# Kernel tuning notes

Measured on AMD Instinct MI355X. Metric: run time of the kernel, lower is better.

Reference implementation:

```python
import math
import jax, jax.numpy as jnp
import numpy as np

B, N, D, H, R = 2, 2048, 1024, 16, 32
DK = D // H  # 64


def _alibi_slopes(n_heads):
    def pow2slopes(n):
        start = 2 ** (-(2 ** (-(math.log2(n) - 3))))
        return [start * (start ** i) for i in range(n)]
    if math.log2(n_heads).is_integer():
        vals = pow2slopes(n_heads)
    else:
        closest = 2 ** math.floor(math.log2(n_heads))
        vals = pow2slopes(closest)
        vals += pow2slopes(2 * closest)[0::2][: n_heads - closest]
    return np.asarray(vals, dtype=np.float32)


def _alibi_bias(n_heads, n_tokens):
    # bias[h, i, j] = -slope[h] * max(j - i, 0)
    i = np.arange(n_tokens)[:, None]
    j = np.arange(n_tokens)[None, :]
    dist = np.clip(j - i, 0, None).astype(np.float32)
    return jnp.asarray(-_alibi_slopes(n_heads)[:, None, None] * dist)  # [H, N, N]


def setup_inputs() -> dict:
    key = jax.random.key(0)
    ks = jax.random.split(key, 6)
    s = 0.02
    return {
        "x": jax.random.normal(ks[0], (B, N, D), dtype=jnp.float32),
        "mask": jnp.zeros((1, 1, N, N), dtype=jnp.float32),
        "W_q": jax.random.normal(ks[1], (D, D), dtype=jnp.float32) * s,
        "W_k": jax.random.normal(ks[2], (D, D), dtype=jnp.float32) * s,
        "W_v": jax.random.normal(ks[3], (D, D), dtype=jnp.float32) * s,
        "U": jax.random.normal(ks[4], (DK, R), dtype=jnp.float32) * (1.0 / math.sqrt(DK)),
        "W_proj": jax.random.normal(ks[5], (D, D), dtype=jnp.float32) * s,
        "rel_bias_tokens": N,
    }


def reference(x, mask, W_q, W_k, W_v, U, W_proj, rel_bias_tokens):
    b, n, d = x.shape
    dk = U.shape[0]
    h = d // dk
    # q/k: Linear (no bias) -> split heads -> low-rank projection via U: [b,h,n,r]
    q = jnp.einsum("bnhd,dr->bhnr", (x @ W_q.T).reshape(b, n, h, dk), U)
    k = jnp.einsum("bnhd,dr->bhnr", (x @ W_k.T).reshape(b, n, h, dk), U)
    v = (x @ W_v.T).reshape(b, n, h, dk).transpose(0, 2, 1, 3)  # [b,h,n,dk]
    # note: scale uses sqrt(dk), not sqrt(r) (custom scale from the module)
    att = jnp.einsum("bhnr,bhmr->bhnm", q, k) / math.sqrt(dk)
    bias = _alibi_bias(h, rel_bias_tokens)  # [h, N_total, N_total]
    att = att + bias[None, :, -n:, :] + mask
    p = jax.nn.softmax(att, axis=-1)
    z = jnp.einsum("bhnm,bhmd->bnhd", p, v).reshape(b, n, h * dk)
    return z @ W_proj.T  # dropout is identity at inference
```

## Files before the change

kernel.cpp:

```cpp
#include <hip/hip_runtime.h>
#include <cstdint>

#define DEV __device__ __forceinline__

typedef __bf16 bf16x8 __attribute__((ext_vector_type(8)));
typedef float f32x4 __attribute__((ext_vector_type(4)));
typedef unsigned short u16x4 __attribute__((ext_vector_type(4)));
typedef unsigned short u16x8 __attribute__((ext_vector_type(8)));
typedef float f32x4v __attribute__((ext_vector_type(4)));

DEV unsigned short f2bf(float f) {
  union { float f; unsigned int u; } v; v.f = f;
  unsigned int r = v.u + 0x7fffu + ((v.u >> 16) & 1u);
  return (unsigned short)(r >> 16);
}

DEV void gl2lds16(const void* g, void* l) {
  __builtin_amdgcn_global_load_lds(
      (const __attribute__((address_space(1))) void*)g,
      (__attribute__((address_space(3))) void*)l, 16, 0, 0);
}

DEV bf16x8 ld8(const unsigned short* p) { return *(const bf16x8*)p; }


__global__ __launch_bounds__(256) void prep(
    const float* __restrict__ x, const float* __restrict__ Wp,
    const float* __restrict__ Wv, const float* __restrict__ Wq,
    const float* __restrict__ Wk, const float* __restrict__ U,
    unsigned short* __restrict__ xb, unsigned short* __restrict__ Wpb,
    unsigned short* __restrict__ Wcat) {
  __shared__ float Us[64 * 32];
  const int bx = blockIdx.x, t = threadIdx.x;
  if (bx < 6144) {
    const float* s; unsigned short* d; int i;
    if (bx < 4096)      { s = x;  d = xb;               i = bx * 256 + t; }
    else if (bx < 5120) { s = Wp; d = Wpb;              i = (bx - 4096) * 256 + t; }
    else                { s = Wv; d = Wcat + 1024*1024; i = (bx - 5120) * 256 + t; }
    f32x4v f = ((const f32x4v*)s)[i];
    u16x4 u;
    u[0] = f2bf(f[0]); u[1] = f2bf(f[1]); u[2] = f2bf(f[2]); u[3] = f2bf(f[3]);
    ((u16x4*)d)[i] = u;
  } else {
    ((f32x4v*)Us)[t] = ((const f32x4v*)U)[t];
    ((f32x4v*)Us)[t + 256] = ((const f32x4v*)U)[t + 256];
    __syncthreads();
    int gid = (bx - 6144) * 256 + t;
    int d = gid & 1023;
    int tmp = gid >> 10;
    int rq = tmp & 7, hh = (tmp >> 3) & 15, qk = tmp >> 7;
    const float* W = qk ? Wk : Wq;
    const float* wp = W + (size_t)(hh * 64) * 1024 + d;
    f32x4v acc = {0.f, 0.f, 0.f, 0.f};
    #pragma unroll 8
    for (int dk = 0; dk < 64; dk++) {
      float wv = wp[(size_t)dk * 1024];
      acc += (*(const f32x4v*)(Us + dk * 32 + rq * 4)) * wv;
    }
    float sc = qk ? 1.0f : 0.18033688011112042f;
    int orow = qk * 512 + hh * 32 + rq * 4;
    #pragma unroll
    for (int i = 0; i < 4; i++)
      Wcat[(size_t)(orow + i) * 1024 + d] = f2bf(acc[i] * sc);
  }
}


template <int OUTF32, int VW, int BM>
__global__ __launch_bounds__(512, 1) void gemm256(
    const unsigned short* __restrict__ A, const unsigned short* __restrict__ Bt,
    void* __restrict__ Cout, unsigned short* __restrict__ Vt,
    int nbx, int Nc, int K) {
  constexpr int MI = BM / 64;
  constexpr int NL = BM / 64 + 2;
  __shared__ __align__(16) unsigned short As[3][BM * 64];
  __shared__ __align__(16) unsigned short Bs[3][128 * 64];
  const int t = threadIdx.x;
  const int w = t >> 6, lane = t & 63;
  const int quad = lane >> 4, l15 = lane & 15;

  const int per = gridDim.x >> 3;
  const int f = blockIdx.x;
  const int wgid = (f & 7) * per + (f >> 3);
  const int by = wgid / nbx, bx = wgid - by * nbx;
  const int row0 = by * BM, col0 = bx * 128;

  const int wr = (w >> 1) * (BM / 4), wc = (w & 1) * 64;

  f32x4 acc[MI][4];
  #pragma unroll
  for (int i = 0; i < MI; i++)
    #pragma unroll
    for (int j = 0; j < 4; j++) acc[i][j] = (f32x4){0.f, 0.f, 0.f, 0.f};

  const int srow = t >> 3;
  const int chnk = t & 7;
  const int swz = (chnk ^ (srow & 7)) * 8;
  const unsigned short* ga = A + (size_t)(row0 + srow) * K + swz;
  const unsigned short* gb = Bt + (size_t)(col0 + srow) * K + swz;
  const int ldsb = w * 512;

  #pragma unroll
  for (int q = 0; q < MI; q++) gl2lds16(ga + (size_t)(q * 64) * K, &As[0][q * 4096 + ldsb]);
  #pragma unroll
  for (int q = 0; q < 2; q++) gl2lds16(gb + (size_t)(q * 64) * K, &Bs[0][q * 4096 + ldsb]);
  if (64 < K) {
    #pragma unroll
    for (int q = 0; q < MI; q++) gl2lds16(ga + (size_t)(q * 64) * K + 64, &As[1][q * 4096 + ldsb]);
    #pragma unroll
    for (int q = 0; q < 2; q++) gl2lds16(gb + (size_t)(q * 64) * K + 64, &Bs[1][q * 4096 + ldsb]);
  }

  int cur = 0, nxt = 2;
  for (int k0 = 0; k0 < K; k0 += 64) {
    if (k0 + 64 < K) {
      if constexpr (NL == 6) asm volatile("s_waitcnt vmcnt(6)" ::: "memory");
      else                   asm volatile("s_waitcnt vmcnt(4)" ::: "memory");
    } else {
      asm volatile("s_waitcnt vmcnt(0)" ::: "memory");
    }
    __builtin_amdgcn_s_barrier();
    __builtin_amdgcn_sched_barrier(0);
    if (k0 + 128 < K) {
      #pragma unroll
      for (int q = 0; q < MI; q++)
        gl2lds16(ga + (size_t)(q * 64) * K + (k0 + 128), &As[nxt][q * 4096 + ldsb]);
      #pragma unroll
      for (int q = 0; q < 2; q++)
        gl2lds16(gb + (size_t)(q * 64) * K + (k0 + 128), &Bs[nxt][q * 4096 + ldsb]);
    }
    #pragma unroll
    for (int s = 0; s < 2; s++) {
      bf16x8 af[MI], bfr[4];
      const int pc = ((s * 4 + quad) ^ (l15 & 7)) << 3;
      #pragma unroll
      for (int i = 0; i < MI; i++)
        af[i] = ld8(&As[cur][(wr + i * 16 + l15) * 64 + pc]);
      #pragma unroll
      for (int j = 0; j < 4; j++)
        bfr[j] = ld8(&Bs[cur][(wc + j * 16 + l15) * 64 + pc]);
      #pragma unroll
      for (int i = 0; i < MI; i++)
        #pragma unroll
        for (int j = 0; j < 4; j++)
          acc[i][j] = __builtin_amdgcn_mfma_f32_16x16x32_bf16(af[i], bfr[j], acc[i][j], 0, 0, 0);
    }
    cur = (cur + 1) % 3; nxt = (nxt + 1) % 3;
  }

  if (VW && bx >= 8) {
    #pragma unroll
    for (int i = 0; i < MI; i++) {
      int r = row0 + wr + i * 16 + quad * 4;
      int bb = r >> 11, n = r & 2047;
      int chunk = (n >> 3) & 15;
      int nbase = (n & ~127) | (n & 4);
      #pragma unroll
      for (int j = 0; j < 4; j++) {
        int vcol = col0 + wc + j * 16 + l15 - 1024;
        int hh = vcol >> 6, dk = vcol & 63;
        int phys = nbase | ((chunk ^ (dk & 15)) << 3);
        u16x4 pk;
        #pragma unroll
        for (int reg = 0; reg < 4; reg++) pk[reg] = f2bf(acc[i][j][reg]);
        *(u16x4*)(Vt + (size_t)((bb * 16 + hh) * 64 + dk) * 2048 + phys) = pk;
      }
    }
  } else {
    #pragma unroll
    for (int i = 0; i < MI; i++)
      #pragma unroll
      for (int j = 0; j < 4; j++) {
        int r = row0 + wr + i * 16 + quad * 4;
        int c = col0 + wc + j * 16 + l15;
        #pragma unroll
        for (int reg = 0; reg < 4; reg++) {
          if (OUTF32) ((float*)Cout)[(size_t)(r + reg) * Nc + c] = acc[i][j][reg];
          else ((unsigned short*)Cout)[(size_t)(r + reg) * Nc + c] = f2bf(acc[i][j][reg]);
        }
      }
  }
}


__global__ __launch_bounds__(256, 2) void flash_attn(
    const unsigned short* __restrict__ QKV, const unsigned short* __restrict__ Vtg,
    unsigned short* __restrict__ Z) {
  __shared__ __align__(16) unsigned short Ps[128 * 128];
  __shared__ __align__(16) unsigned short Ks[2][128 * 32];
  __shared__ __align__(16) unsigned short Vs[2][64 * 128];

  const int f = blockIdx.x;
  const int xcd = f & 7, slot = f >> 3;
  int rk = (slot < 32) ? slot : 95 - slot;
  const int set = xcd >> 1;
  const int b = xcd & 1;
  const unsigned hpack = (set == 0) ? 0x0D0A0400u : (set == 1) ? 0x0C0B0601u
                        : (set == 2) ? 0x0F090502u : 0x0E080703u;
  const unsigned dpack = (set == 0) ? 0x0B040101u : (set == 1) ? 0x08060101u
                        : (set == 2) ? 0x15030101u : 0x0F020201u;
  int h = 0, qt = 0, done = 0;
  #pragma unroll
  for (int c = 16; c >= 2; --c) {
    #pragma unroll
    for (int a = 0; a < 4; ++a) {
      int dh = (int)((dpack >> (8 * a)) & 0xFFu);
      int cnt, qv;
      if (c == 16) { cnt = (dh + 1 > 16) ? 16 : dh + 1; qv = 15 - rk; }
      else         { qv = c - 1 - dh; cnt = (qv >= 0) ? 1 : 0; }
      int take = (done == 0) && (rk < cnt);
      if (take) { h = (int)((hpack >> (8 * a)) & 0xFFu); qt = qv; done = 1; }
      if (!done) rk -= cnt;
    }
  }

  const int t = threadIdx.x;
  const int w = t >> 6, lane = t & 63;
  const int quad = lane >> 4, l15 = lane & 15;
  const int srow = t >> 2;
  const int swz = ((t & 3) ^ ((srow >> 1) & 3)) * 8;
  const int xr = l15 & 7, qh = quad >> 1, qlo = quad & 1;
  const int kchnk = (quad ^ ((l15 >> 1) & 3)) << 3;

  const float slope2 = exp2f(-0.5f * (float)(h + 1)) * 1.4426950408889634f;
  const float slope16 = slope2 * 16.0f;
  int ktend = qt + (int)((15.0f / slope2 + 127.0f) * 0.0078125f);
  if (ktend > 15) ktend = 15;

  const unsigned short* Qg = QKV + (size_t)(b * 2048 + qt * 128) * 1024 + h * 32;
  const unsigned short* Kg = QKV + (size_t)(b * 2048) * 1024 + 512 + h * 32;
  const unsigned short* Vg = Vtg + (size_t)((b * 16 + h) * 64) * 2048;

  gl2lds16(Qg + (size_t)srow * 1024 + swz, &Ks[1][(w * 16) * 32]);
  gl2lds16(Qg + (size_t)(64 + srow) * 1024 + swz, &Ks[1][(64 + w * 16) * 32]);
  gl2lds16(Kg + (size_t)srow * 1024 + swz, &Ks[0][(w * 16) * 32]);
  gl2lds16(Kg + (size_t)(64 + srow) * 1024 + swz, &Ks[0][(64 + w * 16) * 32]);
  #pragma unroll
  for (int c = 0; c < 4; c++)
    gl2lds16(Vg + (size_t)(c * 16 + (t >> 4)) * 2048 + (t & 15) * 8,
             &Vs[0][(c * 16 + w * 4) * 128]);
  __syncthreads();
  bf16x8 qf[2];
  #pragma unroll
  for (int rg = 0; rg < 2; rg++)
    qf[rg] = ld8(&Ks[1][(w * 32 + rg * 16 + l15) * 32 + kchnk]);

  f32x4 o[2][4];
  f32x4 lacc[2];
  #pragma unroll
  for (int rg = 0; rg < 2; rg++) {
    lacc[rg] = (f32x4){0.f, 0.f, 0.f, 0.f};
    #pragma unroll
    for (int j = 0; j < 4; j++) o[rg][j] = (f32x4){0.f, 0.f, 0.f, 0.f};
  }
  bf16x8 onesf;
  #pragma unroll
  for (int i = 0; i < 8; i++) onesf[i] = (__bf16)1.0f;

  f32x4 base0[2];
  int dbase0[2];
  #pragma unroll
  for (int rg = 0; rg < 2; rg++) {
    #pragma unroll
    for (int r = 0; r < 4; r++)
      base0[rg][r] = slope2 * (float)(w * 32 + rg * 16 + l15 - quad * 4 - r);
    dbase0[rg] = quad * 4 - w * 32 - rg * 16 - l15;
  }

  unsigned short* pst0 = Ps + (w * 32 + l15) * 128 + qlo * 4;
  unsigned short* pst1 = pst0 + 16 * 128;
  const f32x4 zero4 = (f32x4){0.f, 0.f, 0.f, 0.f};

  for (int kt = 0; kt <= ktend; kt++) {
    __syncthreads();
    const unsigned short* ksc = Ks[kt & 1];
    const unsigned short* vsc = Vs[kt & 1];
    if (kt < ktend) {
      unsigned short* ksn = Ks[(kt + 1) & 1];
      unsigned short* vsn = Vs[(kt + 1) & 1];
      gl2lds16(Kg + (size_t)((kt + 1) * 128 + srow) * 1024 + swz, &ksn[(w * 16) * 32]);
      gl2lds16(Kg + (size_t)((kt + 1) * 128 + 64 + srow) * 1024 + swz,
               &ksn[(64 + w * 16) * 32]);
      #pragma unroll
      for (int c = 0; c < 4; c++)
        gl2lds16(Vg + (size_t)(c * 16 + (t >> 4)) * 2048 + (kt + 1) * 128 + (t & 15) * 8,
                 &vsn[(c * 16 + w * 4) * 128]);
    }

    f32x4 s[2][8];
    if (kt > qt) {
      float off = slope2 * 128.0f * (float)(kt - qt);
      f32x4 bline[2];
      #pragma unroll
      for (int rg = 0; rg < 2; rg++)
        #pragma unroll
        for (int r = 0; r < 4; r++) bline[rg][r] = base0[rg][r] - off;
      __builtin_amdgcn_s_setprio(1);
      #pragma unroll
      for (int ct = 0; ct < 8; ct++) {
        bf16x8 kf = ld8(&ksc[(ct * 16 + l15) * 32 + kchnk]);
        float cc = slope16 * (float)ct;
        #pragma unroll
        for (int rg = 0; rg < 2; rg++) {
          f32x4 ci;
          ci[0] = bline[rg][0] - cc; ci[1] = bline[rg][1] - cc;
          ci[2] = bline[rg][2] - cc; ci[3] = bline[rg][3] - cc;
          s[rg][ct] = __builtin_amdgcn_mfma_f32_16x16x32_bf16(kf, qf[rg], ci, 0, 0, 0);
        }
      }
      __builtin_amdgcn_s_setprio(0);
    } else {
      __builtin_amdgcn_s_setprio(1);
      #pragma unroll
      for (int ct = 0; ct < 8; ct++) {
        bf16x8 kf = ld8(&ksc[(ct * 16 + l15) * 32 + kchnk]);
        #pragma unroll
        for (int rg = 0; rg < 2; rg++)
          s[rg][ct] = __builtin_amdgcn_mfma_f32_16x16x32_bf16(kf, qf[rg], zero4, 0, 0, 0);
      }
      __builtin_amdgcn_s_setprio(0);
      if (kt == qt) {
        #pragma unroll
        for (int rg = 0; rg < 2; rg++)
          #pragma unroll
          for (int ct = 0; ct < 8; ct++)
            #pragma unroll
            for (int r = 0; r < 4; r++) {
              float d = (float)(ct * 16 + dbase0[rg] + r);
              s[rg][ct][r] += fminf(-slope2 * d, 0.0f);
            }
      }
    }

    #pragma unroll
    for (int rg = 0; rg < 2; rg++) {
      unsigned short* pst = rg ? pst1 : pst0;
      #pragma unroll
      for (int ct = 0; ct < 8; ct++) {
        u16x4 pk;
        #pragma unroll
        for (int r = 0; r < 4; r++) {
          union { float f; unsigned u; } pu;
          pu.f = __builtin_amdgcn_exp2f(s[rg][ct][r]);
          pk[r] = (unsigned short)(pu.u >> 16);
        }
        *(u16x4*)(pst + (((ct * 2 + qh) ^ xr) << 3)) = pk;
      }
    }

    __builtin_amdgcn_s_setprio(1);
    #pragma unroll
    for (int ks = 0; ks < 4; ks++) {
      bf16x8 pf0 = ld8(&Ps[(w * 32 + l15) * 128 + (((ks * 4 + quad) ^ xr) << 3)]);
      bf16x8 pf1 = ld8(&Ps[(w * 32 + 16 + l15) * 128 + (((ks * 4 + quad) ^ xr) << 3)]);
      lacc[0] = __builtin_amdgcn_mfma_f32_16x16x32_bf16(onesf, pf0, lacc[0], 0, 0, 0);
      lacc[1] = __builtin_amdgcn_mfma_f32_16x16x32_bf16(onesf, pf1, lacc[1], 0, 0, 0);
      #pragma unroll
      for (int j = 0; j < 4; j++) {
        bf16x8 vf = ld8(&vsc[(j * 16 + l15) * 128 + (((ks * 4 + quad) ^ l15) << 3)]);
        o[0][j] = __builtin_amdgcn_mfma_f32_16x16x32_bf16(vf, pf0, o[0][j], 0, 0, 0);
        o[1][j] = __builtin_amdgcn_mfma_f32_16x16x32_bf16(vf, pf1, o[1][j], 0, 0, 0);
      }
    }
    __builtin_amdgcn_s_setprio(0);
  }

  #pragma unroll
  for (int rg = 0; rg < 2; rg++) {
    float linv = 1.0f / lacc[rg][0];
    size_t zrow = ((size_t)(b * 2048 + qt * 128 + w * 32 + rg * 16 + l15)) * 1024 + h * 64;
    #pragma unroll
    for (int j = 0; j < 4; j++) {
      u16x4 v4;
      #pragma unroll
      for (int reg = 0; reg < 4; reg++) v4[reg] = f2bf(o[rg][j][reg] * linv);
      *(u16x4*)(Z + zrow + j * 16 + quad * 4) = v4;
    }
  }
}


extern "C" void kernel_launch(void* const* d_in, const int* in_sizes, int n_in,
                              void* d_out, int out_size, void* d_ws, size_t ws_size,
                              hipStream_t stream) {
  const float* x  = (const float*)d_in[0];
  const float* Wq = (const float*)d_in[2];
  const float* Wk = (const float*)d_in[3];
  const float* Wv = (const float*)d_in[4];
  const float* U  = (const float*)d_in[5];
  const float* Wp = (const float*)d_in[6];
  float* out = (float*)d_out;

  char* ws = (char*)d_ws;
  unsigned short* xb   = (unsigned short*)(ws);
  unsigned short* Wcat = (unsigned short*)(ws + 8u * 1024 * 1024);
  unsigned short* Wpb  = (unsigned short*)(ws + 12u * 1024 * 1024);
  unsigned short* QKV  = (unsigned short*)(ws + 14u * 1024 * 1024);
  unsigned short* Zb   = (unsigned short*)(ws + 22u * 1024 * 1024);
  unsigned short* Vtg  = (unsigned short*)(ws + 30u * 1024 * 1024);

  prep<<<7168, 256, 0, stream>>>(x, Wp, Wv, Wq, Wk, U, xb, Wpb, Wcat);
  gemm256<0, 1, 256><<<256, 512, 0, stream>>>(xb, Wcat, QKV, Vtg, 16, 1024, 1024);
  flash_attn<<<512, 256, 0, stream>>>(QKV, Vtg, Zb);
  gemm256<1, 0, 128><<<256, 512, 0, stream>>>(Zb, Wpb, out, nullptr, 8, 1024, 1024);
}
```

Before: 180.9 us.

## Read K and V fragments directly from global memory instead of LDS staging

Drops the double-buffered LDS staging of the K and V tiles, along with the per-iteration block barrier. Each wave now loads its Q, K and V MFMA fragments straight from global memory. The score computation is also restructured to loop over row groups one at a time, which shrinks the live score registers. This removes LDS traffic and synchronisation, but every wave now fetches the full K and V tile on its own, and without prefetch the global load latency is exposed inside the loop.

```diff
diff --git a/kernel.cpp b/kernel.cpp
--- a/kernel.cpp
+++ b/kernel.cpp
@@ -187,8 +187,6 @@
     const unsigned short* __restrict__ QKV, const unsigned short* __restrict__ Vtg,
     unsigned short* __restrict__ Z) {
   __shared__ __align__(16) unsigned short Ps[128 * 128];
-  __shared__ __align__(16) unsigned short Ks[2][128 * 32];
-  __shared__ __align__(16) unsigned short Vs[2][64 * 128];
 
   const int f = blockIdx.x;
   const int xcd = f & 7, slot = f >> 3;
@@ -217,10 +215,7 @@
   const int t = threadIdx.x;
   const int w = t >> 6, lane = t & 63;
   const int quad = lane >> 4, l15 = lane & 15;
-  const int srow = t >> 2;
-  const int swz = ((t & 3) ^ ((srow >> 1) & 3)) * 8;
   const int xr = l15 & 7, qh = quad >> 1, qlo = quad & 1;
-  const int kchnk = (quad ^ ((l15 >> 1) & 3)) << 3;
 
   const float slope2 = exp2f(-0.5f * (float)(h + 1)) * 1.4426950408889634f;
   const float slope16 = slope2 * 16.0f;
@@ -231,19 +226,10 @@
   const unsigned short* Kg = QKV + (size_t)(b * 2048) * 1024 + 512 + h * 32;
   const unsigned short* Vg = Vtg + (size_t)((b * 16 + h) * 64) * 2048;
 
-  gl2lds16(Qg + (size_t)srow * 1024 + swz, &Ks[1][(w * 16) * 32]);
-  gl2lds16(Qg + (size_t)(64 + srow) * 1024 + swz, &Ks[1][(64 + w * 16) * 32]);
-  gl2lds16(Kg + (size_t)srow * 1024 + swz, &Ks[0][(w * 16) * 32]);
-  gl2lds16(Kg + (size_t)(64 + srow) * 1024 + swz, &Ks[0][(64 + w * 16) * 32]);
-  #pragma unroll
-  for (int c = 0; c < 4; c++)
-    gl2lds16(Vg + (size_t)(c * 16 + (t >> 4)) * 2048 + (t & 15) * 8,
-             &Vs[0][(c * 16 + w * 4) * 128]);
-  __syncthreads();
   bf16x8 qf[2];
   #pragma unroll
   for (int rg = 0; rg < 2; rg++)
-    qf[rg] = ld8(&Ks[1][(w * 32 + rg * 16 + l15) * 32 + kchnk]);
+    qf[rg] = ld8(Qg + (size_t)(w * 32 + rg * 16 + l15) * 1024 + quad * 8);
 
   f32x4 o[2][4];
   f32x4 lacc[2];
@@ -268,80 +254,57 @@
   }
 
   unsigned short* pst0 = Ps + (w * 32 + l15) * 128 + qlo * 4;
-  unsigned short* pst1 = pst0 + 16 * 128;
   const f32x4 zero4 = (f32x4){0.f, 0.f, 0.f, 0.f};
 
   for (int kt = 0; kt <= ktend; kt++) {
-    __syncthreads();
-    const unsigned short* ksc = Ks[kt & 1];
-    const unsigned short* vsc = Vs[kt & 1];
-    if (kt < ktend) {
-      unsigned short* ksn = Ks[(kt + 1) & 1];
-      unsigned short* vsn = Vs[(kt + 1) & 1];
-      gl2lds16(Kg + (size_t)((kt + 1) * 128 + srow) * 1024 + swz, &ksn[(w * 16) * 32]);
-      gl2lds16(Kg + (size_t)((kt + 1) * 128 + 64 + srow) * 1024 + swz,
-               &ksn[(64 + w * 16) * 32]);
-      #pragma unroll
-      for (int c = 0; c < 4; c++)
-        gl2lds16(Vg + (size_t)(c * 16 + (t >> 4)) * 2048 + (kt + 1) * 128 + (t & 15) * 8,
-                 &vsn[(c * 16 + w * 4) * 128]);
-    }
-
-    f32x4 s[2][8];
-    if (kt > qt) {
-      float off = slope2 * 128.0f * (float)(kt - qt);
-      f32x4 bline[2];
-      #pragma unroll
-      for (int rg = 0; rg < 2; rg++)
-        #pragma unroll
-        for (int r = 0; r < 4; r++) bline[rg][r] = base0[rg][r] - off;
-      __builtin_amdgcn_s_setprio(1);
-      #pragma unroll
-      for (int ct = 0; ct < 8; ct++) {
-        bf16x8 kf = ld8(&ksc[(ct * 16 + l15) * 32 + kchnk]);
-        float cc = slope16 * (float)ct;
-        #pragma unroll
-        for (int rg = 0; rg < 2; rg++) {
+    const unsigned short* kbase = Kg + (size_t)(kt * 128 + l15) * 1024 + quad * 8;
+
+    #pragma unroll
+    for (int rg = 0; rg < 2; rg++) {
+      f32x4 s[8];
+      if (kt > qt) {
+        float off = slope2 * 128.0f * (float)(kt - qt);
+        f32x4 bline;
+        #pragma unroll
+        for (int r = 0; r < 4; r++) bline[r] = base0[rg][r] - off;
+        __builtin_amdgcn_s_setprio(1);
+        #pragma unroll
+        for (int ct = 0; ct < 8; ct++) {
+          bf16x8 kf = ld8(kbase + (size_t)(ct * 16) * 1024);
+          float cc = slope16 * (float)ct;
           f32x4 ci;
-          ci[0] = bline[rg][0] - cc; ci[1] = bline[rg][1] - cc;
-          ci[2] = bline[rg][2] - cc; ci[3] = bline[rg][3] - cc;
-          s[rg][ct] = __builtin_amdgcn_mfma_f32_16x16x32_bf16(kf, qf[rg], ci, 0, 0, 0);
-        }
-      }
-      __builtin_amdgcn_s_setprio(0);
-    } else {
-      __builtin_amdgcn_s_setprio(1);
-      #pragma unroll
-      for (int ct = 0; ct < 8; ct++) {
-        bf16x8 kf = ld8(&ksc[(ct * 16 + l15) * 32 + kchnk]);
-        #pragma unroll
-        for (int rg = 0; rg < 2; rg++)
-          s[rg][ct] = __builtin_amdgcn_mfma_f32_16x16x32_bf16(kf, qf[rg], zero4, 0, 0, 0);
-      }
-      __builtin_amdgcn_s_setprio(0);
-      if (kt == qt) {
-        #pragma unroll
-        for (int rg = 0; rg < 2; rg++)
+          ci[0] = bline[0] - cc; ci[1] = bline[1] - cc;
+          ci[2] = bline[2] - cc; ci[3] = bline[3] - cc;
+          s[ct] = __builtin_amdgcn_mfma_f32_16x16x32_bf16(kf, qf[rg], ci, 0, 0, 0);
+        }
+        __builtin_amdgcn_s_setprio(0);
+      } else {
+        __builtin_amdgcn_s_setprio(1);
+        #pragma unroll
+        for (int ct = 0; ct < 8; ct++) {
+          bf16x8 kf = ld8(kbase + (size_t)(ct * 16) * 1024);
+          s[ct] = __builtin_amdgcn_mfma_f32_16x16x32_bf16(kf, qf[rg], zero4, 0, 0, 0);
+        }
+        __builtin_amdgcn_s_setprio(0);
+        if (kt == qt) {
           #pragma unroll
           for (int ct = 0; ct < 8; ct++)
             #pragma unroll
             for (int r = 0; r < 4; r++) {
               float d = (float)(ct * 16 + dbase0[rg] + r);
-              s[rg][ct][r] += fminf(-slope2 * d, 0.0f);
+              s[ct][r] += fminf(-slope2 * d, 0.0f);
             }
-      }
-    }
-
-    #pragma unroll
-    for (int rg = 0; rg < 2; rg++) {
-      unsigned short* pst = rg ? pst1 : pst0;
+        }
+      }
+
+      unsigned short* pst = pst0 + rg * (16 * 128);
       #pragma unroll
       for (int ct = 0; ct < 8; ct++) {
         u16x4 pk;
         #pragma unroll
         for (int r = 0; r < 4; r++) {
           union { float f; unsigned u; } pu;
-          pu.f = __builtin_amdgcn_exp2f(s[rg][ct][r]);
+          pu.f = __builtin_amdgcn_exp2f(s[ct][r]);
           pk[r] = (unsigned short)(pu.u >> 16);
         }
         *(u16x4*)(pst + (((ct * 2 + qh) ^ xr) << 3)) = pk;
@@ -357,7 +320,8 @@
       lacc[1] = __builtin_amdgcn_mfma_f32_16x16x32_bf16(onesf, pf1, lacc[1], 0, 0, 0);
       #pragma unroll
       for (int j = 0; j < 4; j++) {
-        bf16x8 vf = ld8(&vsc[(j * 16 + l15) * 128 + (((ks * 4 + quad) ^ l15) << 3)]);
+        bf16x8 vf = ld8(Vg + (size_t)(j * 16 + l15) * 2048 + kt * 128 +
+                        (((ks * 4 + quad) ^ l15) << 3));
         o[0][j] = __builtin_amdgcn_mfma_f32_16x16x32_bf16(vf, pf0, o[0][j], 0, 0, 0);
         o[1][j] = __builtin_amdgcn_mfma_f32_16x16x32_bf16(vf, pf1, o[1][j], 0, 0, 0);
       }
```

After: 217.1 us. 20.0% more time.
